# Kernel tuning notes

Measured on AMD Instinct MI355X. Metric: run time of the kernel, lower is better.

Reference implementation:

```python
import jax, jax.numpy as jnp
import numpy as np

T, B, I, H, O = 1024, 256, 256, 256, 256


def setup_inputs() -> dict:
    key = jax.random.key(0)
    ks = jax.random.split(key, 12)
    s = 0.01  # init scale matching np.random.normal(0, 0.01)
    return {
        "x_steps": jax.random.normal(ks[0], (T, B, I), dtype=jnp.float32),
        "h": jnp.zeros((B, H), dtype=jnp.float32),
        "w_xr": s * jax.random.normal(ks[1], (I, H), dtype=jnp.float32),
        "w_hr": s * jax.random.normal(ks[2], (H, H), dtype=jnp.float32),
        "b_r": jnp.zeros((H,), dtype=jnp.float32),
        "w_xz": s * jax.random.normal(ks[3], (I, H), dtype=jnp.float32),
        "w_hz": s * jax.random.normal(ks[4], (H, H), dtype=jnp.float32),
        "b_z": jnp.zeros((H,), dtype=jnp.float32),
        "w_xh": s * jax.random.normal(ks[5], (I, H), dtype=jnp.float32),
        "w_hh": s * jax.random.normal(ks[6], (H, H), dtype=jnp.float32),
        "b_h": jnp.zeros((H,), dtype=jnp.float32),
        "w_out": s * jax.random.normal(ks[7], (H, O), dtype=jnp.float32),
        "b_out": jnp.zeros((O,), dtype=jnp.float32),
    }


def reference(x_steps, h, w_xr, w_hr, b_r, w_xz, w_hz, b_z,
              w_xh, w_hh, b_h, w_out, b_out):
    # Precompute all input projections in one batched GEMM per gate: [T,B,H]
    xr = jnp.einsum('tbi,ih->tbh', x_steps, w_xr) + b_r
    xz = jnp.einsum('tbi,ih->tbh', x_steps, w_xz) + b_z
    xh = jnp.einsum('tbi,ih->tbh', x_steps, w_xh) + b_h

    def step(h, xs):
        xr_t, xz_t, xh_t = xs
        r = jax.nn.sigmoid(xr_t + h @ w_hr)
        z = jax.nn.sigmoid(xz_t + h @ w_hz)
        cand = jnp.tanh(xh_t + (r * h) @ w_hh)
        h_new = h * z + (1.0 - z) * cand
        # NOTE: original emits matmul(cand, W_out)+b, using the candidate,
        # not the updated hidden state -- replicate faithfully.
        out = cand @ w_out + b_out
        return h_new, out

    h_final, outs = jax.lax.scan(step, h, (xr, xz, xh))  # outs: [T,B,O]
    return outs.reshape(T * B, O), h_final  # torch.cat(result_list, dim=0)
```

## Files before the change

### kernel.cpp

```cpp
#include <hip/hip_runtime.h>


typedef unsigned short u16t;
typedef unsigned int   u32t;
typedef short  s16x8 __attribute__((ext_vector_type(8)));
typedef float  f32x4 __attribute__((ext_vector_type(4)));
typedef float  f32v4 __attribute__((ext_vector_type(4)));
typedef u32t   u32x2 __attribute__((ext_vector_type(2)));

#define GBYTES 134217728ull
#define L2E 1.4426950408889634f

#define BAR_LDS() asm volatile("s_waitcnt lgkmcnt(0)\n\ts_barrier" ::: "memory")
#define PIN(v) asm volatile("" : "+v"(v))

__device__ __forceinline__ float lo_f(u32t u) {
  return __builtin_bit_cast(float, u << 16);
}
__device__ __forceinline__ float hi_f(u32t u) {
  return __builtin_bit_cast(float, u & 0xffff0000u);
}
__device__ __forceinline__ u32t f2bf(float f) {
  u32t u = __builtin_bit_cast(u32t, f);
  return (u + 0x7fffu + ((u >> 16) & 1u)) >> 16;
}
__device__ __forceinline__ u32t cvtpk(float lo, float hi) {
  u32t r;
  asm("v_cvt_pk_bf16_f32 %0, %1, %2" : "=v"(r) : "v"(lo), "v"(hi));
  return r;
}
__device__ __forceinline__ f32x4 MF(s16x8 a, s16x8 b, f32x4 c) {
  return __builtin_amdgcn_mfma_f32_16x16x32_bf16(a, b, c, 0, 0, 0);
}
__device__ __forceinline__ float sigm2(float y) {
  return __builtin_amdgcn_rcpf(1.0f + __builtin_amdgcn_exp2f(-y));
}
__device__ __forceinline__ float tanh2(float y) {
  return fmaf(-2.0f, __builtin_amdgcn_rcpf(__builtin_amdgcn_exp2f(y) + 1.0f), 1.0f);
}

__global__ void pack_w(const float* __restrict__ wxr, const float* __restrict__ wxz,
                       const float* __restrict__ wxh, const float* __restrict__ whr,
                       const float* __restrict__ whz, const float* __restrict__ whh,
                       const float* __restrict__ wout, u16t* __restrict__ dst) {
  int e = blockIdx.x * 256 + threadIdx.x;
  int mat = e >> 16, i = e & 65535;
  const float* src = mat == 0 ? wxr : mat == 1 ? wxz : mat == 2 ? wxh
                   : mat == 3 ? whr : mat == 4 ? whz : mat == 5 ? whh : wout;
  float sc = (mat == 2 || mat == 5) ? 2.0f * L2E : (mat == 6 ? 1.0f : L2E);
  int j = i & 7, lane = (i >> 3) & 63, ks = (i >> 9) & 7, nb = i >> 12;
  int k = ks * 32 + (lane >> 4) * 8 + j;
  int n = nb * 16 + (lane & 15);
  dst[e] = (u16t)f2bf(src[k * 256 + n] * sc);
}

__global__ __launch_bounds__(512, 2) void gru_xproj(
    const float* __restrict__ x, const u16t* __restrict__ wpack,
    const float* __restrict__ br, const float* __restrict__ bz,
    const float* __restrict__ bh,
    u16t* __restrict__ xr_p, u16t* __restrict__ xz_p, u16t* __restrict__ xh_p) {
  __shared__ __align__(128) u16t xt[16384];
  const int tid = threadIdx.x, bid = blockIdx.x;
  const int t = bid >> 2, b0 = (bid & 3) * 64;
  const float* xrow = x + ((size_t)t * 256 + b0) * 256;
#pragma unroll
  for (int c = 0; c < 8; ++c) {
    int f4 = c * 512 + tid;
    f32v4 v = ((const f32v4*)xrow)[f4];
    u32t lo = f2bf(v[0]) | (f2bf(v[1]) << 16);
    u32t hi = f2bf(v[2]) | (f2bf(v[3]) << 16);
    int row = f4 >> 6, c8 = (f4 & 63) * 8;
    int off = (row * 512 + c8) ^ ((row & 7) << 4);
    u32x2 vv; vv[0] = lo; vv[1] = hi;
    *(u32x2*)((char*)xt + off) = vv;
  }
  __syncthreads();
  const int lane = tid & 63, w = tid >> 6;
  const int m2 = w & 1, cg = w >> 1;
  const int arow = m2 * 32 + (lane & 15);
  const int abase = arow * 512 + (lane >> 4) * 16;
  const int asw = (lane & 7) << 4;
  const f32x4 Z = {0.f, 0.f, 0.f, 0.f};
  f32x4 acc[2][12];
#pragma unroll
  for (int s = 0; s < 2; ++s)
#pragma unroll
    for (int p = 0; p < 12; ++p) acc[s][p] = Z;
#pragma unroll
  for (int ks = 0; ks < 8; ++ks) {
    s16x8 a0 = *(const s16x8*)((char*)xt + ((abase + ks * 64) ^ asw));
    s16x8 a1 = *(const s16x8*)((char*)xt + ((abase + 16 * 512 + ks * 64) ^ asw));
#pragma unroll
    for (int p = 0; p < 12; ++p) {
      int pj = cg * 12 + p;
      int gate = pj >> 4, nb = pj & 15;
      const s16x8* wb = (const s16x8*)wpack + gate * 8192;
      s16x8 b = wb[(nb * 8 + ks) * 64 + lane];
      acc[0][p] = MF(a0, b, acc[0][p]);
      acc[1][p] = MF(a1, b, acc[1][p]);
    }
  }
#pragma unroll
  for (int p = 0; p < 12; ++p) {
    int pj = cg * 12 + p;
    int gate = pj >> 4, nb = pj & 15;
    const float* bp = gate == 0 ? br : gate == 1 ? bz : bh;
    float bs = (gate == 2) ? 2.0f * L2E : L2E;
    float bv = bp[nb * 16 + (lane & 15)] * bs;
    u16t* op = gate == 0 ? xr_p : gate == 1 ? xz_p : xh_p;
#pragma unroll
    for (int s = 0; s < 2; ++s) {
      int wg = (b0 >> 4) + m2 * 2 + s;
      u32t lo = f2bf(acc[s][p][0] + bv) | (f2bf(acc[s][p][1] + bv) << 16);
      u32t hi = f2bf(acc[s][p][2] + bv) | (f2bf(acc[s][p][3] + bv) << 16);
      size_t off = (((size_t)t * 16 + wg) * 16 + nb) * 64 + lane;
      u32x2 vv; vv[0] = lo; vv[1] = hi;
      ((u32x2*)op)[off] = vv;
    }
  }
}

#define OFFSW(row, colx2) (((row) * 512 + (colx2)) ^ (((row) & 7) << 4))
#define LDA_HB(ks) (*(const s16x8*)((char*)hb + ((aoff + (ks) * 64) ^ asw)))
#define LDA_RH(ks) (*(const s16x8*)((char*)rh + ((aoff + (ks) * 64) ^ asw)))
#define ZLOAD(buf, ks) do { buf[0] = pz[(ks) * 64]; buf[1] = pz[(ks) * 64 + 512]; } while (0)
#define G1_STEP(buf, ks) do { s16x8 a_ = LDA_HB(ks); \
    ar0 = MF(a_, whr_r[0][ks], ar0); ar1 = MF(a_, whr_r[1][ks], ar1); \
    az0 = MF(a_, buf[0], az0);       az1 = MF(a_, buf[1], az1); } while (0)

__global__ __launch_bounds__(512, 2) void gru_scan(
    const float* __restrict__ h0, const u16t* __restrict__ wpack,
    const u16t* __restrict__ xr_p, const u16t* __restrict__ xz_p,
    const u16t* __restrict__ xh_p, u16t* __restrict__ cand_p,
    float* __restrict__ hout) {
  __shared__ __align__(128) u16t hb[4096];
  __shared__ __align__(128) u16t rh[4096];
  const int tid = threadIdx.x, lane = tid & 63, w = tid >> 6;
  const int wg = blockIdx.x;
  const int rlo = (lane >> 4) * 4;
  const int cA = w * 32 + (lane & 15);

  float hr_[2][4];
#pragma unroll
  for (int c = 0; c < 2; ++c)
#pragma unroll
    for (int j = 0; j < 4; ++j)
      hr_[c][j] = h0[(size_t)(wg * 16 + rlo + j) * 256 + cA + c * 16];
#pragma unroll
  for (int c = 0; c < 2; ++c)
#pragma unroll
    for (int j = 0; j < 4; ++j)
      *(u16t*)((char*)hb + OFFSW(rlo + j, (cA + c * 16) * 2)) = (u16t)f2bf(hr_[c][j]);
  __syncthreads();

  const s16x8* pz = (const s16x8*)wpack + 4 * 8192 + w * 1024 + lane;
  const int aoff = (lane & 15) * 512 + (lane >> 4) * 16;
  const int asw = (lane & 7) << 4;

  s16x8 whr_r[2][8], whh_r[2][8];
  {
    const s16x8* prw = (const s16x8*)wpack + 3 * 8192;
    const s16x8* phw = (const s16x8*)wpack + 5 * 8192;
#pragma unroll
    for (int c = 0; c < 2; ++c)
#pragma unroll
      for (int ks = 0; ks < 8; ++ks) {
        int fo = ((2 * w + c) * 8 + ks) * 64 + lane;
        whr_r[c][ks] = prw[fo]; PIN(whr_r[c][ks]);
        whh_r[c][ks] = phw[fo]; PIN(whh_r[c][ks]);
      }
  }

  const size_t xoff = (size_t)(wg * 16 + 2 * w) * 64 + lane;
  const u32x2* PXR = (const u32x2*)xr_p;
  const u32x2* PXZ = (const u32x2*)xz_p;
  const u32x2* PXH = (const u32x2*)xh_p;
  u32x2* SXH = (u32x2*)cand_p;

  u32x2 vxr0 = PXR[xoff], vxr1 = PXR[xoff + 64];
  u32x2 vxz0 = PXZ[xoff], vxz1 = PXZ[xoff + 64];
  u32x2 vxh0 = PXH[xoff], vxh1 = PXH[xoff + 64];

  s16x8 bA[2], bB[2];
  ZLOAD(bA, 0);
  ZLOAD(bB, 1);

  for (int t = 0; t < 1024; ++t) {
    f32x4 ar0, ar1, az0, az1;
    ar0[0] = lo_f(vxr0[0]); ar0[1] = hi_f(vxr0[0]); ar0[2] = lo_f(vxr0[1]); ar0[3] = hi_f(vxr0[1]);
    ar1[0] = lo_f(vxr1[0]); ar1[1] = hi_f(vxr1[0]); ar1[2] = lo_f(vxr1[1]); ar1[3] = hi_f(vxr1[1]);
    az0[0] = lo_f(vxz0[0]); az0[1] = hi_f(vxz0[0]); az0[2] = lo_f(vxz0[1]); az0[3] = hi_f(vxz0[1]);
    az1[0] = lo_f(vxz1[0]); az1[1] = hi_f(vxz1[0]); az1[2] = lo_f(vxz1[1]); az1[3] = hi_f(vxz1[1]);

    G1_STEP(bA, 0); ZLOAD(bA, 2);
    G1_STEP(bB, 1); ZLOAD(bB, 3);
    G1_STEP(bA, 2); ZLOAD(bA, 4);
    G1_STEP(bB, 3); ZLOAD(bB, 5);
    G1_STEP(bA, 4); ZLOAD(bA, 6);
    G1_STEP(bB, 5); ZLOAD(bB, 7);
    G1_STEP(bA, 6);
    G1_STEP(bB, 7);

    float r_[2][4];
    r_[0][0] = sigm2(ar0[0]); r_[0][1] = sigm2(ar0[1]); r_[0][2] = sigm2(ar0[2]); r_[0][3] = sigm2(ar0[3]);
    r_[1][0] = sigm2(ar1[0]); r_[1][1] = sigm2(ar1[1]); r_[1][2] = sigm2(ar1[2]); r_[1][3] = sigm2(ar1[3]);

#pragma unroll
    for (int c = 0; c < 2; ++c) {
      u32t p01 = cvtpk(r_[c][0] * hr_[c][0], r_[c][1] * hr_[c][1]);
      u32t p23 = cvtpk(r_[c][2] * hr_[c][2], r_[c][3] * hr_[c][3]);
      *(u16t*)((char*)rh + OFFSW(rlo + 0, (cA + c * 16) * 2)) = (u16t)p01;
      *(u16t*)((char*)rh + OFFSW(rlo + 1, (cA + c * 16) * 2)) = (u16t)(p01 >> 16);
      *(u16t*)((char*)rh + OFFSW(rlo + 2, (cA + c * 16) * 2)) = (u16t)p23;
      *(u16t*)((char*)rh + OFFSW(rlo + 3, (cA + c * 16) * 2)) = (u16t)(p23 >> 16);
    }
    BAR_LDS();

    float z_[2][4];
    z_[0][0] = sigm2(az0[0]); z_[0][1] = sigm2(az0[1]); z_[0][2] = sigm2(az0[2]); z_[0][3] = sigm2(az0[3]);
    z_[1][0] = sigm2(az1[0]); z_[1][1] = sigm2(az1[1]); z_[1][2] = sigm2(az1[2]); z_[1][3] = sigm2(az1[3]);

    f32x4 ac0, ac1;
    ac0[0] = lo_f(vxh0[0]); ac0[1] = hi_f(vxh0[0]); ac0[2] = lo_f(vxh0[1]); ac0[3] = hi_f(vxh0[1]);
    ac1[0] = lo_f(vxh1[0]); ac1[1] = hi_f(vxh1[0]); ac1[2] = lo_f(vxh1[1]); ac1[3] = hi_f(vxh1[1]);

    {
      size_t onext = xoff + (size_t)(t < 1023 ? t + 1 : t) * 16384;
      vxr0 = PXR[onext]; vxr1 = PXR[onext + 64];
      vxz0 = PXZ[onext]; vxz1 = PXZ[onext + 64];
      vxh0 = PXH[onext]; vxh1 = PXH[onext + 64];
    }

#pragma unroll
    for (int ks = 0; ks < 8; ++ks) {
      s16x8 a_ = LDA_RH(ks);
      ac0 = MF(a_, whh_r[0][ks], ac0);
      ac1 = MF(a_, whh_r[1][ks], ac1);
    }

    float cd[2][4];
    cd[0][0] = tanh2(ac0[0]); cd[0][1] = tanh2(ac0[1]); cd[0][2] = tanh2(ac0[2]); cd[0][3] = tanh2(ac0[3]);
    cd[1][0] = tanh2(ac1[0]); cd[1][1] = tanh2(ac1[1]); cd[1][2] = tanh2(ac1[2]); cd[1][3] = tanh2(ac1[3]);

    size_t ocur = xoff + (size_t)t * 16384;
    u32x2 s0, s1;
    s0[0] = cvtpk(cd[0][0], cd[0][1]); s0[1] = cvtpk(cd[0][2], cd[0][3]);
    s1[0] = cvtpk(cd[1][0], cd[1][1]); s1[1] = cvtpk(cd[1][2], cd[1][3]);
    SXH[ocur] = s0;
    SXH[ocur + 64] = s1;

#pragma unroll
    for (int c = 0; c < 2; ++c) {
#pragma unroll
      for (int j = 0; j < 4; ++j)
        hr_[c][j] = fmaf(z_[c][j], hr_[c][j] - cd[c][j], cd[c][j]);
      u32t p01 = cvtpk(hr_[c][0], hr_[c][1]);
      u32t p23 = cvtpk(hr_[c][2], hr_[c][3]);
      *(u16t*)((char*)hb + OFFSW(rlo + 0, (cA + c * 16) * 2)) = (u16t)p01;
      *(u16t*)((char*)hb + OFFSW(rlo + 1, (cA + c * 16) * 2)) = (u16t)(p01 >> 16);
      *(u16t*)((char*)hb + OFFSW(rlo + 2, (cA + c * 16) * 2)) = (u16t)p23;
      *(u16t*)((char*)hb + OFFSW(rlo + 3, (cA + c * 16) * 2)) = (u16t)(p23 >> 16);
    }

    ZLOAD(bA, 0);
    ZLOAD(bB, 1);
    BAR_LDS();
  }
#pragma unroll
  for (int c = 0; c < 2; ++c)
#pragma unroll
    for (int j = 0; j < 4; ++j)
      hout[(size_t)(wg * 16 + rlo + j) * 256 + cA + c * 16] = hr_[c][j];
}

__global__ __launch_bounds__(1024, 4) void gru_out(
    const u16t* __restrict__ cand_p, const u16t* __restrict__ wpack,
    const float* __restrict__ bout, float* __restrict__ out) {
  __shared__ __align__(128) u16t cm[16384];
  const int tid = threadIdx.x, bid = blockIdx.x;
  const int t = bid >> 2, q = bid & 3, b0 = q * 64;
  const u32x2* src = (const u32x2*)cand_p + ((size_t)t * 16 + q * 4) * 1024;
#pragma unroll
  for (int it = 0; it < 4; ++it) {
    int i = it * 1024 + tid;
    u32x2 v = src[i];
    int wg_l = i >> 10, nb = (i >> 6) & 15, ls = i & 63;
    int brow = wg_l * 16 + (ls >> 4) * 4;
    int hc2 = (nb * 16 + (ls & 15)) * 2;
    u16t ev[4] = {(u16t)(v[0] & 0xffff), (u16t)(v[0] >> 16),
                  (u16t)(v[1] & 0xffff), (u16t)(v[1] >> 16)};
#pragma unroll
    for (int j = 0; j < 4; ++j)
      *(u16t*)((char*)cm + OFFSW(brow + j, hc2)) = ev[j];
  }
  __syncthreads();
  const int lane = tid & 63, w = tid >> 6;
  const int mt = w & 3, nbs = (w >> 2) * 4;
  const int arow = mt * 16 + (lane & 15);
  const int abase = arow * 512 + (lane >> 4) * 16;
  const int asw = (lane & 7) << 4;
  const f32x4 Z = {0.f, 0.f, 0.f, 0.f};
  f32x4 acc[4] = {Z, Z, Z, Z};
  const s16x8* wo = (const s16x8*)wpack + 6 * 8192;
#pragma unroll
  for (int ks = 0; ks < 8; ++ks) {
    s16x8 a = *(const s16x8*)((char*)cm + ((abase + ks * 64) ^ asw));
#pragma unroll
    for (int p = 0; p < 4; ++p)
      acc[p] = MF(a, wo[((nbs + p) * 8 + ks) * 64 + lane], acc[p]);
  }
#pragma unroll
  for (int p = 0; p < 4; ++p) {
    int col = (nbs + p) * 16 + (lane & 15);
    float bv = bout[col];
    size_t rb = (size_t)t * 256 + b0 + mt * 16 + (lane >> 4) * 4;
#pragma unroll
    for (int j = 0; j < 4; ++j)
      out[(rb + j) * 256 + col] = acc[p][j] + bv;
  }
}

extern "C" void kernel_launch(void* const* d_in, const int* in_sizes, int n_in,
                              void* d_out, int out_size, void* d_ws, size_t ws_size,
                              hipStream_t stream) {
  const float* x    = (const float*)d_in[0];
  const float* h0   = (const float*)d_in[1];
  const float* wxr  = (const float*)d_in[2];
  const float* whr  = (const float*)d_in[3];
  const float* br   = (const float*)d_in[4];
  const float* wxz  = (const float*)d_in[5];
  const float* whz  = (const float*)d_in[6];
  const float* bz   = (const float*)d_in[7];
  const float* wxh  = (const float*)d_in[8];
  const float* whh  = (const float*)d_in[9];
  const float* bh   = (const float*)d_in[10];
  const float* wout = (const float*)d_in[11];
  const float* bout = (const float*)d_in[12];

  float* out  = (float*)d_out;
  u16t* wpack = (u16t*)d_ws;
  u16t* xh_p  = (u16t*)((char*)d_ws + (1u << 20));
  u16t* xr_p  = (u16t*)d_out;
  u16t* xz_p  = (u16t*)((char*)d_out + GBYTES);
  float* hout = (float*)((char*)d_out + 2 * GBYTES);

  pack_w<<<1792, 256, 0, stream>>>(wxr, wxz, wxh, whr, whz, whh, wout, wpack);
  gru_xproj<<<4096, 512, 0, stream>>>(x, wpack, br, bz, bh, xr_p, xz_p, xh_p);
  gru_scan<<<16, 512, 0, stream>>>(h0, wpack, xr_p, xz_p, xh_p, xh_p, hout);
  gru_out<<<4096, 1024, 0, stream>>>(xh_p, wpack, bout, out);
}
```

Measured before the change: 2.622 ms.

## Fuse scan and output projection into persistent producer-consumer kernel

Merges the recurrent scan and the output GEMM into one launch. 16 blocks run the scan and publish progress every 16 timesteps through atomic flags, while 112 consumer blocks poll those flags and compute cand@W_out for finished timesteps. The goal is to hide the output projection and its large fp32 output writes behind the latency-bound scan instead of running them afterwards. The xr/xz buffers are interleaved inside the output buffer so consumers only overwrite regions the scan has already read. This adds spin-polling and memory traffic that may compete with the scan's critical path, and its correctness depends on the aliasing and fence ordering.

```diff
diff --git a/kernel.cpp b/kernel.cpp
--- a/kernel.cpp
+++ b/kernel.cpp
@@ -8,8 +8,8 @@
 typedef float  f32v4 __attribute__((ext_vector_type(4)));
 typedef u32t   u32x2 __attribute__((ext_vector_type(2)));
 
-#define GBYTES 134217728ull
 #define L2E 1.4426950408889634f
+#define NCONS 112
 
 #define BAR_LDS() asm volatile("s_waitcnt lgkmcnt(0)\n\ts_barrier" ::: "memory")
 #define PIN(v) asm volatile("" : "+v"(v))
@@ -42,7 +42,9 @@
 __global__ void pack_w(const float* __restrict__ wxr, const float* __restrict__ wxz,
                        const float* __restrict__ wxh, const float* __restrict__ whr,
                        const float* __restrict__ whz, const float* __restrict__ whh,
-                       const float* __restrict__ wout, u16t* __restrict__ dst) {
+                       const float* __restrict__ wout, u16t* __restrict__ dst,
+                       int* __restrict__ prog) {
+  if (blockIdx.x == 0 && threadIdx.x < 16) prog[threadIdx.x] = 0;
   int e = blockIdx.x * 256 + threadIdx.x;
   int mat = e >> 16, i = e & 65535;
   const float* src = mat == 0 ? wxr : mat == 1 ? wxz : mat == 2 ? wxh
@@ -113,7 +115,9 @@
       int wg = (b0 >> 4) + m2 * 2 + s;
       u32t lo = f2bf(acc[s][p][0] + bv) | (f2bf(acc[s][p][1] + bv) << 16);
       u32t hi = f2bf(acc[s][p][2] + bv) | (f2bf(acc[s][p][3] + bv) << 16);
-      size_t off = (((size_t)t * 16 + wg) * 16 + nb) * 64 + lane;
+      size_t off = (gate == 2)
+          ? (size_t)t * 16384 + wg * 1024 + nb * 64 + lane
+          : (size_t)t * 32768 + wg * 1024 + nb * 64 + lane;
       u32x2 vv; vv[0] = lo; vv[1] = hi;
       ((u32x2*)op)[off] = vv;
     }
@@ -128,195 +132,236 @@
     ar0 = MF(a_, whr_r[0][ks], ar0); ar1 = MF(a_, whr_r[1][ks], ar1); \
     az0 = MF(a_, buf[0], az0);       az1 = MF(a_, buf[1], az1); } while (0)
 
-__global__ __launch_bounds__(512, 2) void gru_scan(
+__global__ __launch_bounds__(512, 2) void gru_fused(
     const float* __restrict__ h0, const u16t* __restrict__ wpack,
     const u16t* __restrict__ xr_p, const u16t* __restrict__ xz_p,
-    const u16t* __restrict__ xh_p, u16t* __restrict__ cand_p,
-    float* __restrict__ hout) {
-  __shared__ __align__(128) u16t hb[4096];
-  __shared__ __align__(128) u16t rh[4096];
+    const u16t* __restrict__ xh_p, u16t* __restrict__ cand_w,
+    const u16t* __restrict__ cand_r, float* __restrict__ hout,
+    int* __restrict__ prog, const float* __restrict__ bout,
+    float* __restrict__ out) {
+  __shared__ __align__(128) u16t smem[16384];
   const int tid = threadIdx.x, lane = tid & 63, w = tid >> 6;
-  const int wg = blockIdx.x;
-  const int rlo = (lane >> 4) * 4;
-  const int cA = w * 32 + (lane & 15);
-
-  float hr_[2][4];
-#pragma unroll
-  for (int c = 0; c < 2; ++c)
-#pragma unroll
-    for (int j = 0; j < 4; ++j)
-      hr_[c][j] = h0[(size_t)(wg * 16 + rlo + j) * 256 + cA + c * 16];
-#pragma unroll
-  for (int c = 0; c < 2; ++c)
-#pragma unroll
-    for (int j = 0; j < 4; ++j)
-      *(u16t*)((char*)hb + OFFSW(rlo + j, (cA + c * 16) * 2)) = (u16t)f2bf(hr_[c][j]);
-  __syncthreads();
-
-  const s16x8* pz = (const s16x8*)wpack + 4 * 8192 + w * 1024 + lane;
-  const int aoff = (lane & 15) * 512 + (lane >> 4) * 16;
-  const int asw = (lane & 7) << 4;
-
-  s16x8 whr_r[2][8], whh_r[2][8];
-  {
-    const s16x8* prw = (const s16x8*)wpack + 3 * 8192;
-    const s16x8* phw = (const s16x8*)wpack + 5 * 8192;
+  const int bid = blockIdx.x;
+
+  if (bid < 16) {
+    u16t* hb = smem;
+    u16t* rh = smem + 4096;
+    const int wg = bid;
+    const int rlo = (lane >> 4) * 4;
+    const int cA = w * 32 + (lane & 15);
+
+    float hr_[2][4];
 #pragma unroll
     for (int c = 0; c < 2; ++c)
 #pragma unroll
-      for (int ks = 0; ks < 8; ++ks) {
-        int fo = ((2 * w + c) * 8 + ks) * 64 + lane;
-        whr_r[c][ks] = prw[fo]; PIN(whr_r[c][ks]);
-        whh_r[c][ks] = phw[fo]; PIN(whh_r[c][ks]);
-      }
-  }
-
-  const size_t xoff = (size_t)(wg * 16 + 2 * w) * 64 + lane;
-  const u32x2* PXR = (const u32x2*)xr_p;
-  const u32x2* PXZ = (const u32x2*)xz_p;
-  const u32x2* PXH = (const u32x2*)xh_p;
-  u32x2* SXH = (u32x2*)cand_p;
-
-  u32x2 vxr0 = PXR[xoff], vxr1 = PXR[xoff + 64];
-  u32x2 vxz0 = PXZ[xoff], vxz1 = PXZ[xoff + 64];
-  u32x2 vxh0 = PXH[xoff], vxh1 = PXH[xoff + 64];
-
-  s16x8 bA[2], bB[2];
-  ZLOAD(bA, 0);
-  ZLOAD(bB, 1);
-
-  for (int t = 0; t < 1024; ++t) {
-    f32x4 ar0, ar1, az0, az1;
-    ar0[0] = lo_f(vxr0[0]); ar0[1] = hi_f(vxr0[0]); ar0[2] = lo_f(vxr0[1]); ar0[3] = hi_f(vxr0[1]);
-    ar1[0] = lo_f(vxr1[0]); ar1[1] = hi_f(vxr1[0]); ar1[2] = lo_f(vxr1[1]); ar1[3] = hi_f(vxr1[1]);
-    az0[0] = lo_f(vxz0[0]); az0[1] = hi_f(vxz0[0]); az0[2] = lo_f(vxz0[1]); az0[3] = hi_f(vxz0[1]);
-    az1[0] = lo_f(vxz1[0]); az1[1] = hi_f(vxz1[0]); az1[2] = lo_f(vxz1[1]); az1[3] = hi_f(vxz1[1]);
-
-    G1_STEP(bA, 0); ZLOAD(bA, 2);
-    G1_STEP(bB, 1); ZLOAD(bB, 3);
-    G1_STEP(bA, 2); ZLOAD(bA, 4);
-    G1_STEP(bB, 3); ZLOAD(bB, 5);
-    G1_STEP(bA, 4); ZLOAD(bA, 6);
-    G1_STEP(bB, 5); ZLOAD(bB, 7);
-    G1_STEP(bA, 6);
-    G1_STEP(bB, 7);
-
-    float r_[2][4];
-    r_[0][0] = sigm2(ar0[0]); r_[0][1] = sigm2(ar0[1]); r_[0][2] = sigm2(ar0[2]); r_[0][3] = sigm2(ar0[3]);
-    r_[1][0] = sigm2(ar1[0]); r_[1][1] = sigm2(ar1[1]); r_[1][2] = sigm2(ar1[2]); r_[1][3] = sigm2(ar1[3]);
-
-#pragma unroll
-    for (int c = 0; c < 2; ++c) {
-      u32t p01 = cvtpk(r_[c][0] * hr_[c][0], r_[c][1] * hr_[c][1]);
-      u32t p23 = cvtpk(r_[c][2] * hr_[c][2], r_[c][3] * hr_[c][3]);
-      *(u16t*)((char*)rh + OFFSW(rlo + 0, (cA + c * 16) * 2)) = (u16t)p01;
-      *(u16t*)((char*)rh + OFFSW(rlo + 1, (cA + c * 16) * 2)) = (u16t)(p01 >> 16);
-      *(u16t*)((char*)rh + OFFSW(rlo + 2, (cA + c * 16) * 2)) = (u16t)p23;
-      *(u16t*)((char*)rh + OFFSW(rlo + 3, (cA + c * 16) * 2)) = (u16t)(p23 >> 16);
-    }
-    BAR_LDS();
-
-    float z_[2][4];
-    z_[0][0] = sigm2(az0[0]); z_[0][1] = sigm2(az0[1]); z_[0][2] = sigm2(az0[2]); z_[0][3] = sigm2(az0[3]);
-    z_[1][0] = sigm2(az1[0]); z_[1][1] = sigm2(az1[1]); z_[1][2] = sigm2(az1[2]); z_[1][3] = sigm2(az1[3]);
-
-    f32x4 ac0, ac1;
-    ac0[0] = lo_f(vxh0[0]); ac0[1] = hi_f(vxh0[0]); ac0[2] = lo_f(vxh0[1]); ac0[3] = hi_f(vxh0[1]);
-    ac1[0] = lo_f(vxh1[0]); ac1[1] = hi_f(vxh1[0]); ac1[2] = lo_f(vxh1[1]); ac1[3] = hi_f(vxh1[1]);
-
+      for (int j = 0; j < 4; ++j)
+        hr_[c][j] = h0[(size_t)(wg * 16 + rlo + j) * 256 + cA + c * 16];
+#pragma unroll
+    for (int c = 0; c < 2; ++c)
+#pragma unroll
+      for (int j = 0; j < 4; ++j)
+        *(u16t*)((char*)hb + OFFSW(rlo + j, (cA + c * 16) * 2)) = (u16t)f2bf(hr_[c][j]);
+    __syncthreads();
+
+    const s16x8* pz = (const s16x8*)wpack + 4 * 8192 + w * 1024 + lane;
+    const int aoff = (lane & 15) * 512 + (lane >> 4) * 16;
+    const int asw = (lane & 7) << 4;
+
+    s16x8 whr_r[2][8], whh_r[2][8];
     {
-      size_t onext = xoff + (size_t)(t < 1023 ? t + 1 : t) * 16384;
-      vxr0 = PXR[onext]; vxr1 = PXR[onext + 64];
-      vxz0 = PXZ[onext]; vxz1 = PXZ[onext + 64];
-      vxh0 = PXH[onext]; vxh1 = PXH[onext + 64];
-    }
-
-#pragma unroll
-    for (int ks = 0; ks < 8; ++ks) {
-      s16x8 a_ = LDA_RH(ks);
-      ac0 = MF(a_, whh_r[0][ks], ac0);
-      ac1 = MF(a_, whh_r[1][ks], ac1);
-    }
-
-    float cd[2][4];
-    cd[0][0] = tanh2(ac0[0]); cd[0][1] = tanh2(ac0[1]); cd[0][2] = tanh2(ac0[2]); cd[0][3] = tanh2(ac0[3]);
-    cd[1][0] = tanh2(ac1[0]); cd[1][1] = tanh2(ac1[1]); cd[1][2] = tanh2(ac1[2]); cd[1][3] = tanh2(ac1[3]);
-
-    size_t ocur = xoff + (size_t)t * 16384;
-    u32x2 s0, s1;
-    s0[0] = cvtpk(cd[0][0], cd[0][1]); s0[1] = cvtpk(cd[0][2], cd[0][3]);
-    s1[0] = cvtpk(cd[1][0], cd[1][1]); s1[1] = cvtpk(cd[1][2], cd[1][3]);
-    SXH[ocur] = s0;
-    SXH[ocur + 64] = s1;
-
-#pragma unroll
-    for (int c = 0; c < 2; ++c) {
-#pragma unroll
-      for (int j = 0; j < 4; ++j)
-        hr_[c][j] = fmaf(z_[c][j], hr_[c][j] - cd[c][j], cd[c][j]);
-      u32t p01 = cvtpk(hr_[c][0], hr_[c][1]);
-      u32t p23 = cvtpk(hr_[c][2], hr_[c][3]);
-      *(u16t*)((char*)hb + OFFSW(rlo + 0, (cA + c * 16) * 2)) = (u16t)p01;
-      *(u16t*)((char*)hb + OFFSW(rlo + 1, (cA + c * 16) * 2)) = (u16t)(p01 >> 16);
-      *(u16t*)((char*)hb + OFFSW(rlo + 2, (cA + c * 16) * 2)) = (u16t)p23;
-      *(u16t*)((char*)hb + OFFSW(rlo + 3, (cA + c * 16) * 2)) = (u16t)(p23 >> 16);
-    }
-
+      const s16x8* prw = (const s16x8*)wpack + 3 * 8192;
+      const s16x8* phw = (const s16x8*)wpack + 5 * 8192;
+#pragma unroll
+      for (int c = 0; c < 2; ++c)
+#pragma unroll
+        for (int ks = 0; ks < 8; ++ks) {
+          int fo = ((2 * w + c) * 8 + ks) * 64 + lane;
+          whr_r[c][ks] = prw[fo]; PIN(whr_r[c][ks]);
+          whh_r[c][ks] = phw[fo]; PIN(whh_r[c][ks]);
+        }
+    }
+
+    const size_t xoffRZ = (size_t)wg * 1024 + w * 128 + lane;
+    const size_t xoffH  = (size_t)wg * 1024 + w * 128 + lane;
+    const u32x2* PXR = (const u32x2*)xr_p;
+    const u32x2* PXZ = (const u32x2*)xz_p;
+    const u32x2* PXH = (const u32x2*)xh_p;
+    u32x2* SXH = (u32x2*)cand_w;
+
+    u32x2 vxr0 = PXR[xoffRZ], vxr1 = PXR[xoffRZ + 64];
+    u32x2 vxz0 = PXZ[xoffRZ], vxz1 = PXZ[xoffRZ + 64];
+    u32x2 vxh0 = PXH[xoffH],  vxh1 = PXH[xoffH + 64];
+
+    s16x8 bA[2], bB[2];
     ZLOAD(bA, 0);
     ZLOAD(bB, 1);
-    BAR_LDS();
-  }
-#pragma unroll
-  for (int c = 0; c < 2; ++c)
-#pragma unroll
-    for (int j = 0; j < 4; ++j)
-      hout[(size_t)(wg * 16 + rlo + j) * 256 + cA + c * 16] = hr_[c][j];
-}
-
-__global__ __launch_bounds__(1024, 4) void gru_out(
-    const u16t* __restrict__ cand_p, const u16t* __restrict__ wpack,
-    const float* __restrict__ bout, float* __restrict__ out) {
-  __shared__ __align__(128) u16t cm[16384];
-  const int tid = threadIdx.x, bid = blockIdx.x;
-  const int t = bid >> 2, q = bid & 3, b0 = q * 64;
-  const u32x2* src = (const u32x2*)cand_p + ((size_t)t * 16 + q * 4) * 1024;
-#pragma unroll
-  for (int it = 0; it < 4; ++it) {
-    int i = it * 1024 + tid;
-    u32x2 v = src[i];
-    int wg_l = i >> 10, nb = (i >> 6) & 15, ls = i & 63;
-    int brow = wg_l * 16 + (ls >> 4) * 4;
-    int hc2 = (nb * 16 + (ls & 15)) * 2;
-    u16t ev[4] = {(u16t)(v[0] & 0xffff), (u16t)(v[0] >> 16),
-                  (u16t)(v[1] & 0xffff), (u16t)(v[1] >> 16)};
-#pragma unroll
-    for (int j = 0; j < 4; ++j)
-      *(u16t*)((char*)cm + OFFSW(brow + j, hc2)) = ev[j];
-  }
-  __syncthreads();
-  const int lane = tid & 63, w = tid >> 6;
-  const int mt = w & 3, nbs = (w >> 2) * 4;
-  const int arow = mt * 16 + (lane & 15);
-  const int abase = arow * 512 + (lane >> 4) * 16;
-  const int asw = (lane & 7) << 4;
-  const f32x4 Z = {0.f, 0.f, 0.f, 0.f};
-  f32x4 acc[4] = {Z, Z, Z, Z};
-  const s16x8* wo = (const s16x8*)wpack + 6 * 8192;
-#pragma unroll
-  for (int ks = 0; ks < 8; ++ks) {
-    s16x8 a = *(const s16x8*)((char*)cm + ((abase + ks * 64) ^ asw));
-#pragma unroll
-    for (int p = 0; p < 4; ++p)
-      acc[p] = MF(a, wo[((nbs + p) * 8 + ks) * 64 + lane], acc[p]);
-  }
-#pragma unroll
-  for (int p = 0; p < 4; ++p) {
-    int col = (nbs + p) * 16 + (lane & 15);
-    float bv = bout[col];
-    size_t rb = (size_t)t * 256 + b0 + mt * 16 + (lane >> 4) * 4;
-#pragma unroll
-    for (int j = 0; j < 4; ++j)
-      out[(rb + j) * 256 + col] = acc[p][j] + bv;
+
+    for (int t = 0; t < 1024; ++t) {
+      f32x4 ar0, ar1, az0, az1;
+      ar0[0] = lo_f(vxr0[0]); ar0[1] = hi_f(vxr0[0]); ar0[2] = lo_f(vxr0[1]); ar0[3] = hi_f(vxr0[1]);
+      ar1[0] = lo_f(vxr1[0]); ar1[1] = hi_f(vxr1[0]); ar1[2] = lo_f(vxr1[1]); ar1[3] = hi_f(vxr1[1]);
+      az0[0] = lo_f(vxz0[0]); az0[1] = hi_f(vxz0[0]); az0[2] = lo_f(vxz0[1]); az0[3] = hi_f(vxz0[1]);
+      az1[0] = lo_f(vxz1[0]); az1[1] = hi_f(vxz1[0]); az1[2] = lo_f(vxz1[1]); az1[3] = hi_f(vxz1[1]);
+
+      G1_STEP(bA, 0); ZLOAD(bA, 2);
+      G1_STEP(bB, 1); ZLOAD(bB, 3);
+      G1_STEP(bA, 2); ZLOAD(bA, 4);
+      G1_STEP(bB, 3); ZLOAD(bB, 5);
+      G1_STEP(bA, 4); ZLOAD(bA, 6);
+      G1_STEP(bB, 5); ZLOAD(bB, 7);
+      G1_STEP(bA, 6);
+      G1_STEP(bB, 7);
+
+      float r_[2][4];
+      r_[0][0] = sigm2(ar0[0]); r_[0][1] = sigm2(ar0[1]); r_[0][2] = sigm2(ar0[2]); r_[0][3] = sigm2(ar0[3]);
+      r_[1][0] = sigm2(ar1[0]); r_[1][1] = sigm2(ar1[1]); r_[1][2] = sigm2(ar1[2]); r_[1][3] = sigm2(ar1[3]);
+
+#pragma unroll
+      for (int c = 0; c < 2; ++c) {
+        u32t p01 = cvtpk(r_[c][0] * hr_[c][0], r_[c][1] * hr_[c][1]);
+        u32t p23 = cvtpk(r_[c][2] * hr_[c][2], r_[c][3] * hr_[c][3]);
+        *(u16t*)((char*)rh + OFFSW(rlo + 0, (cA + c * 16) * 2)) = (u16t)p01;
+        *(u16t*)((char*)rh + OFFSW(rlo + 1, (cA + c * 16) * 2)) = (u16t)(p01 >> 16);
+        *(u16t*)((char*)rh + OFFSW(rlo + 2, (cA + c * 16) * 2)) = (u16t)p23;
+        *(u16t*)((char*)rh + OFFSW(rlo + 3, (cA + c * 16) * 2)) = (u16t)(p23 >> 16);
+      }
+      BAR_LDS();
+
+      float z_[2][4];
+      z_[0][0] = sigm2(az0[0]); z_[0][1] = sigm2(az0[1]); z_[0][2] = sigm2(az0[2]); z_[0][3] = sigm2(az0[3]);
+      z_[1][0] = sigm2(az1[0]); z_[1][1] = sigm2(az1[1]); z_[1][2] = sigm2(az1[2]); z_[1][3] = sigm2(az1[3]);
+
+      f32x4 ac0, ac1;
+      ac0[0] = lo_f(vxh0[0]); ac0[1] = hi_f(vxh0[0]); ac0[2] = lo_f(vxh0[1]); ac0[3] = hi_f(vxh0[1]);
+      ac1[0] = lo_f(vxh1[0]); ac1[1] = hi_f(vxh1[0]); ac1[2] = lo_f(vxh1[1]); ac1[3] = hi_f(vxh1[1]);
+
+      {
+        int tn = t < 1023 ? t + 1 : t;
+        size_t oRZ = xoffRZ + (size_t)tn * 32768;
+        size_t oH  = xoffH + (size_t)tn * 16384;
+        vxr0 = PXR[oRZ]; vxr1 = PXR[oRZ + 64];
+        vxz0 = PXZ[oRZ]; vxz1 = PXZ[oRZ + 64];
+        vxh0 = PXH[oH];  vxh1 = PXH[oH + 64];
+      }
+
+#pragma unroll
+      for (int ks = 0; ks < 8; ++ks) {
+        s16x8 a_ = LDA_RH(ks);
+        ac0 = MF(a_, whh_r[0][ks], ac0);
+        ac1 = MF(a_, whh_r[1][ks], ac1);
+      }
+
+      float cd[2][4];
+      cd[0][0] = tanh2(ac0[0]); cd[0][1] = tanh2(ac0[1]); cd[0][2] = tanh2(ac0[2]); cd[0][3] = tanh2(ac0[3]);
+      cd[1][0] = tanh2(ac1[0]); cd[1][1] = tanh2(ac1[1]); cd[1][2] = tanh2(ac1[2]); cd[1][3] = tanh2(ac1[3]);
+
+      size_t ocur = xoffH + (size_t)t * 16384;
+      u32x2 s0, s1;
+      s0[0] = cvtpk(cd[0][0], cd[0][1]); s0[1] = cvtpk(cd[0][2], cd[0][3]);
+      s1[0] = cvtpk(cd[1][0], cd[1][1]); s1[1] = cvtpk(cd[1][2], cd[1][3]);
+      SXH[ocur] = s0;
+      SXH[ocur + 64] = s1;
+
+#pragma unroll
+      for (int c = 0; c < 2; ++c) {
+#pragma unroll
+        for (int j = 0; j < 4; ++j)
+          hr_[c][j] = fmaf(z_[c][j], hr_[c][j] - cd[c][j], cd[c][j]);
+        u32t p01 = cvtpk(hr_[c][0], hr_[c][1]);
+        u32t p23 = cvtpk(hr_[c][2], hr_[c][3]);
+        *(u16t*)((char*)hb + OFFSW(rlo + 0, (cA + c * 16) * 2)) = (u16t)p01;
+        *(u16t*)((char*)hb + OFFSW(rlo + 1, (cA + c * 16) * 2)) = (u16t)(p01 >> 16);
+        *(u16t*)((char*)hb + OFFSW(rlo + 2, (cA + c * 16) * 2)) = (u16t)p23;
+        *(u16t*)((char*)hb + OFFSW(rlo + 3, (cA + c * 16) * 2)) = (u16t)(p23 >> 16);
+      }
+
+      ZLOAD(bA, 0);
+      ZLOAD(bB, 1);
+      BAR_LDS();
+
+      if ((t & 15) == 15) {
+        __threadfence();
+        __syncthreads();
+        if (tid == 0)
+          __hip_atomic_store(prog + wg, t + 1, __ATOMIC_RELAXED,
+                             __HIP_MEMORY_SCOPE_AGENT);
+      }
+    }
+#pragma unroll
+    for (int c = 0; c < 2; ++c)
+#pragma unroll
+      for (int j = 0; j < 4; ++j)
+        hout[(size_t)(wg * 16 + rlo + j) * 256 + cA + c * 16] = hr_[c][j];
+
+  } else {
+    u16t* cm = smem;
+    const int cid = bid - 16;
+    const s16x8* wo = (const s16x8*)wpack + 6 * 8192;
+    const int mt = w & 3, nbs = (w >> 2) * 8;
+    const int arow = mt * 16 + (lane & 15);
+    const int abase = arow * 512 + (lane >> 4) * 16;
+    const int asw = (lane & 7) << 4;
+    const f32x4 Z = {0.f, 0.f, 0.f, 0.f};
+    int lastmn = 0;
+
+    for (int tile = cid; tile < 4096; tile += NCONS) {
+      const int t = tile >> 2, q = tile & 3;
+      const int need = t + 1;
+      if (lastmn < need) {
+        if (tid == 0) {
+          int mn;
+          for (;;) {
+            mn = 1 << 30;
+#pragma unroll
+            for (int s = 0; s < 16; ++s)
+              mn = min(mn, __hip_atomic_load(prog + s, __ATOMIC_RELAXED,
+                                             __HIP_MEMORY_SCOPE_AGENT));
+            if (mn >= need) break;
+            __builtin_amdgcn_s_sleep(8);
+            __builtin_amdgcn_s_sleep(8);
+            __builtin_amdgcn_s_sleep(8);
+            __builtin_amdgcn_s_sleep(8);
+          }
+          *(int*)cm = mn;
+        }
+        __syncthreads();
+        lastmn = *(volatile int*)cm;
+        __syncthreads();
+      }
+      const u32x2* src = (const u32x2*)cand_r + ((size_t)t * 16 + q * 4) * 1024;
+#pragma unroll
+      for (int it = 0; it < 8; ++it) {
+        int i = it * 512 + tid;
+        u32x2 v = src[i];
+        int wg_l = i >> 10, nb = (i >> 6) & 15, ls = i & 63;
+        int brow = wg_l * 16 + (ls >> 4) * 4;
+        int hc2 = (nb * 16 + (ls & 15)) * 2;
+        u16t ev[4] = {(u16t)(v[0] & 0xffff), (u16t)(v[0] >> 16),
+                      (u16t)(v[1] & 0xffff), (u16t)(v[1] >> 16)};
+#pragma unroll
+        for (int j = 0; j < 4; ++j)
+          *(u16t*)((char*)cm + OFFSW(brow + j, hc2)) = ev[j];
+      }
+      __syncthreads();
+      f32x4 acc[8] = {Z, Z, Z, Z, Z, Z, Z, Z};
+#pragma unroll
+      for (int ks = 0; ks < 8; ++ks) {
+        s16x8 a = *(const s16x8*)((char*)cm + ((abase + ks * 64) ^ asw));
+#pragma unroll
+        for (int p = 0; p < 8; ++p)
+          acc[p] = MF(a, wo[((nbs + p) * 8 + ks) * 64 + lane], acc[p]);
+      }
+#pragma unroll
+      for (int p = 0; p < 8; ++p) {
+        int col = (nbs + p) * 16 + (lane & 15);
+        float bv = bout[col];
+        size_t rb = (size_t)t * 256 + q * 64 + mt * 16 + (lane >> 4) * 4;
+#pragma unroll
+        for (int j = 0; j < 4; ++j)
+          out[(rb + j) * 256 + col] = acc[p][j] + bv;
+      }
+      __syncthreads();
+    }
   }
 }
 
@@ -339,13 +384,14 @@
 
   float* out  = (float*)d_out;
   u16t* wpack = (u16t*)d_ws;
+  int*  prog  = (int*)((char*)d_ws + 917504);
   u16t* xh_p  = (u16t*)((char*)d_ws + (1u << 20));
   u16t* xr_p  = (u16t*)d_out;
-  u16t* xz_p  = (u16t*)((char*)d_out + GBYTES);
-  float* hout = (float*)((char*)d_out + 2 * GBYTES);
-
-  pack_w<<<1792, 256, 0, stream>>>(wxr, wxz, wxh, whr, whz, whh, wout, wpack);
+  u16t* xz_p  = (u16t*)d_out + 65536;
+  float* hout = (float*)((char*)d_out + 268435456ull);
+
+  pack_w<<<1792, 256, 0, stream>>>(wxr, wxz, wxh, whr, whz, whh, wout, wpack, prog);
   gru_xproj<<<4096, 512, 0, stream>>>(x, wpack, br, bz, bh, xr_p, xz_p, xh_p);
-  gru_scan<<<16, 512, 0, stream>>>(h0, wpack, xr_p, xz_p, xh_p, xh_p, hout);
-  gru_out<<<4096, 1024, 0, stream>>>(xh_p, wpack, bout, out);
-}
+  gru_fused<<<16 + NCONS, 512, 0, stream>>>(h0, wpack, xr_p, xz_p, xh_p,
+                                            xh_p, xh_p, hout, prog, bout, out);
+}
```

New measurement: 2.772 ms. 5.7% more time.
